# Performance work log

Hardware: AMD Instinct MI355X
Metric: run time of the kernel (lower is better)

The kernel has to match this reference:

```python
import jax, jax.numpy as jnp
import numpy as np
from jax import lax


def setup_inputs() -> dict:
    key = jax.random.key(0)
    kx, kw = jax.random.split(key)
    x = jax.random.normal(kx, (8, 32, 16, 160, 160), dtype=jnp.float32)
    # xavier-normal-ish init (scale irrelevant to correctness testing)
    weights = jax.random.normal(kw, (32, 32, 1, 3, 3), dtype=jnp.float32) * 0.1
    return {"x": x, "weights": weights}


def reference(x, weights):
    # per-(out_ch, in_ch) scale: mean |w| over kernel dims (2,3,4), detached
    scale = lax.stop_gradient(jnp.mean(jnp.abs(weights), axis=(2, 3, 4), keepdims=True))
    binary_no_grad = scale * jnp.sign(weights)          # {+-scale}
    clipped = jnp.clip(weights, -1.0, 1.0)
    # straight-through estimator: value = binary_no_grad, grad flows via clipped
    binary_weights = lax.stop_gradient(binary_no_grad - clipped) + clipped
    out = lax.conv_general_dilated(
        x, binary_weights,
        window_strides=(1, 1, 1),
        padding=((0, 0), (1, 1), (1, 1)),
        rhs_dilation=(1, 1, 1),
        dimension_numbers=("NCDHW", "OIDHW", "NCDHW"),
        feature_group_count=1,
    )
    return out
```

## Files before the change

kernel.cpp:

```cpp
#include <hip/hip_runtime.h>
#include <stdint.h>


typedef _Float16 half8  __attribute__((ext_vector_type(8)));
typedef float    floatx4 __attribute__((ext_vector_type(4)));

#define DHW 409600
#define HW  25600
#define RING_SLOT_B 10240
#define RING_B      40960
#define SCR_SLOT_B  20480
#define LDS_TOTAL   81920

__device__ __forceinline__ int w1s(int w1) { return w1 ^ ((w1 >> 2) & 1); }
__device__ __forceinline__ int f2v(int w1) { return ((w1 >> 1) ^ (w1 >> 3)) & 3; }

typedef const __attribute__((address_space(1))) uint32_t* gas1;
typedef __attribute__((address_space(3))) uint32_t* las3;
__device__ __forceinline__ void gld16(const void* g, void* l) {
    __builtin_amdgcn_global_load_lds((gas1)g, (las3)l, 16, 0, 0);
}
#define VMCNT(N) do { asm volatile("s_waitcnt vmcnt(" #N ")" ::: "memory"); \
                      __builtin_amdgcn_sched_barrier(0); } while (0)
__device__ __forceinline__ void barrier_raw() {
    __builtin_amdgcn_sched_barrier(0);
    asm volatile("s_waitcnt lgkmcnt(0)" ::: "memory");
    __builtin_amdgcn_s_barrier();
    __builtin_amdgcn_sched_barrier(0);
}

__global__ void bnn_wprep_kernel(const float* __restrict__ w,
                                 _Float16* __restrict__ ws) {
    const int tid = threadIdx.x;
    #pragma unroll
    for (int p4 = 0; p4 < 4; ++p4) {
        const int oi = tid * 4 + p4;
        const int o  = oi >> 5;
        const int i  = oi & 31;
        const float* wp = w + oi * 9;
        float s = 0.f;
        #pragma unroll
        for (int t = 0; t < 9; ++t) s += fabsf(wp[t]);
        s *= (1.f / 9.f);
        const int l = ((i >> 3) << 4) | (o & 15);
        const int p = o >> 4;
        const int j = i & 7;
        #pragma unroll
        for (int t = 0; t < 9; ++t) {
            const float v  = wp[t];
            const float sg = (v > 0.f) ? 1.f : ((v < 0.f) ? -1.f : 0.f);
            ws[((t * 2 + p) * 64 + l) * 8 + j] = (_Float16)(s * sg);
        }
    }
}

__global__ __launch_bounds__(320) void bnn_conv3d_dma(
        const float* __restrict__ x, const _Float16* __restrict__ ws,
        float* __restrict__ out) {
    extern __shared__ __align__(16) char lds[];

    const int tid  = threadIdx.x;
    const int lane = tid & 63;
    const int wv   = tid >> 6;

    const int bid = blockIdx.x;
    const int hc  = bid & 3;
    const int d   = (bid >> 2) & 15;
    const int n   = bid >> 6;
    const int h0  = hc * 40;

    const float* qb[4];
    {
        const int chl = lane >> 3;
        const int wl  = (lane & 7) * 4;
        #pragma unroll
        for (int q = 0; q < 4; ++q)
            qb[q] = x + (size_t)(n * 32 + q * 8 + chl) * DHW + d * HW + wv * 32 + wl;
    }

    half8 wf0[9], wf1[9];
    {
        const half8* fb = (const half8*)ws;
        #pragma unroll
        for (int t = 0; t < 9; ++t) {
            wf0[t] = fb[(t * 2 + 0) * 64 + lane];
            wf1[t] = fb[(t * 2 + 1) * 64 + lane];
        }
    }
    asm volatile("s_waitcnt vmcnt(0)" ::: "memory");
    __builtin_amdgcn_sched_barrier(0);

    const int pcell = 32 * wv + (lane >> 1);
    const int w1p   = w1s(pcell);
    const int wloc  = w1p - wv * 32;
    const int chb   = (lane & 1) * 16;
    int soff[16];
    #pragma unroll
    for (int c = 0; c < 16; ++c) {
        const int ch = chb + c;
        soff[c] = (wv * 4 + (ch >> 3)) * 1024 + ((ch & 7) * 8 + (wloc >> 2)) * 16
                + (wloc & 3) * 4;
    }
    const int f2p = f2v(pcell);
    const int rb0 = pcell * 64 + ((((lane & 1) * 2)     ^ f2p) * 16);
    const int rb1 = pcell * 64 + ((((lane & 1) * 2 + 1) ^ f2p) * 16);

    const int s16 = lane & 15, kgr = lane >> 4;
    int rdo[2][3];
    #pragma unroll
    for (int gi = 0; gi < 2; ++gi)
        #pragma unroll
        for (int kw = 0; kw < 3; ++kw) {
            int wq = (2 * wv + gi) * 16 + s16 + kw - 1;
            wq = wq < 0 ? 0 : (wq > 159 ? 159 : wq);
            rdo[gi][kw] = (w1s(wq) * 32 + ((kgr ^ f2v(wq)) * 8)) * 2;
        }
    const bool okA = (wv * 32 + s16 - 1) >= 0;
    const bool okB = (wv * 32 + 16 + s16 + 1) < 160;
    float* ob = out + (size_t)(n * 32 + s16) * DHW + d * HW + wv * 32 + kgr * 4;

    auto DMA = [&](int r) {
        int h = h0 - 1 + r; h = h < 0 ? 0 : (h > 159 ? 159 : h);
        char* dst = lds + RING_B + (r & 1) * SCR_SLOT_B + wv * 4096;
        #pragma unroll
        for (int q = 0; q < 4; ++q)
            gld16(qb[q] + h * 160, dst + q * 1024);
        __builtin_amdgcn_sched_barrier(0);
    };
    auto PACK = [&](int r) {
        const int hr = h0 - 1 + r;
        const char* sl = lds + RING_B + (r & 1) * SCR_SLOT_B;
        char* rg = lds + (r & 3) * RING_SLOT_B;
        half8 o0 = {}, o1 = {};
        if (hr >= 0 && hr < 160) {
            float f[16];
            #pragma unroll
            for (int c = 0; c < 16; ++c) f[c] = *(const float*)(sl + soff[c]);
            #pragma unroll
            for (int c = 0; c < 8; ++c) { o0[c] = (_Float16)f[c]; o1[c] = (_Float16)f[c + 8]; }
        }
        *(half8*)(rg + rb0) = o0;
        *(half8*)(rg + rb1) = o1;
    };
    auto COMPUTE = [&](int t) {
        const half8 zh = {};
        #pragma unroll
        for (int gi = 0; gi < 2; ++gi) {
            floatx4 a0 = {0.f, 0.f, 0.f, 0.f};
            floatx4 a1 = {0.f, 0.f, 0.f, 0.f};
            #pragma unroll
            for (int kh = 0; kh < 3; ++kh) {
                const char* sb = lds + ((t + kh) & 3) * RING_SLOT_B;
                #pragma unroll
                for (int kw = 0; kw < 3; ++kw) {
                    half8 a = *(const half8*)(sb + rdo[gi][kw]);
                    if (gi == 0 && kw == 0) a = okA ? a : zh;
                    if (gi == 1 && kw == 2) a = okB ? a : zh;
                    const int tp = kh * 3 + kw;
                    a0 = __builtin_amdgcn_mfma_f32_16x16x32_f16(a, wf0[tp], a0, 0, 0, 0);
                    a1 = __builtin_amdgcn_mfma_f32_16x16x32_f16(a, wf1[tp], a1, 0, 0, 0);
                }
            }
            float* op = ob + (size_t)(h0 + t) * 160 + gi * 16;
            *(floatx4*)op = a0;
            *(floatx4*)(op + (size_t)16 * DHW) = a1;
        }
    };

    DMA(0); DMA(1);
    VMCNT(4);  PACK(0);
    barrier_raw(); DMA(2);
    VMCNT(4);  PACK(1);
    barrier_raw(); DMA(3);
    VMCNT(4);  PACK(2); barrier_raw(); DMA(4); COMPUTE(0);
    VMCNT(8);  PACK(3); barrier_raw(); DMA(5); COMPUTE(1);
    for (int t = 2; t <= 37; ++t) {
        VMCNT(12); PACK(t + 2); barrier_raw(); DMA(t + 4); COMPUTE(t);
    }
    VMCNT(12); PACK(40); barrier_raw(); COMPUTE(38);
    VMCNT(8);  PACK(41); barrier_raw(); COMPUTE(39);
}

extern "C" void kernel_launch(void* const* d_in, const int* in_sizes, int n_in,
                              void* d_out, int out_size, void* d_ws, size_t ws_size,
                              hipStream_t stream) {
    const float* x = (const float*)d_in[0];
    const float* w = (const float*)d_in[1];
    float* out = (float*)d_out;
    _Float16* ws = (_Float16*)d_ws;
    bnn_wprep_kernel<<<dim3(1), dim3(256), 0, stream>>>(w, ws);
    (void)hipFuncSetAttribute((const void*)&bnn_conv3d_dma,
                              hipFuncAttributeMaxDynamicSharedMemorySize, LDS_TOTAL);
    bnn_conv3d_dma<<<dim3(512), dim3(320), LDS_TOTAL, stream>>>(x, ws, out);
}
```

Measured before the change: 188.7 us.

## Fuse weight binarization into conv kernel and halve grid with taller row tiles

Removes the separate single-block weight-prep kernel. Each conv block now binarizes the weights itself into LDS while its first input-row DMAs are in flight, then loads its MFMA weight fragments from LDS. The grid is halved to 256 blocks, each covering 80 output rows instead of 40, which cuts halo row reloads and per-block prologue cost. The trade-offs are redundant weight preparation in every block and fewer resident blocks per CU, so less latency hiding.

```diff
diff --git a/kernel.cpp b/kernel.cpp
--- a/kernel.cpp
+++ b/kernel.cpp
@@ -29,45 +29,20 @@
     __builtin_amdgcn_sched_barrier(0);
 }
 
-__global__ void bnn_wprep_kernel(const float* __restrict__ w,
-                                 _Float16* __restrict__ ws) {
-    const int tid = threadIdx.x;
-    #pragma unroll
-    for (int p4 = 0; p4 < 4; ++p4) {
-        const int oi = tid * 4 + p4;
-        const int o  = oi >> 5;
-        const int i  = oi & 31;
-        const float* wp = w + oi * 9;
-        float s = 0.f;
-        #pragma unroll
-        for (int t = 0; t < 9; ++t) s += fabsf(wp[t]);
-        s *= (1.f / 9.f);
-        const int l = ((i >> 3) << 4) | (o & 15);
-        const int p = o >> 4;
-        const int j = i & 7;
-        #pragma unroll
-        for (int t = 0; t < 9; ++t) {
-            const float v  = wp[t];
-            const float sg = (v > 0.f) ? 1.f : ((v < 0.f) ? -1.f : 0.f);
-            ws[((t * 2 + p) * 64 + l) * 8 + j] = (_Float16)(s * sg);
-        }
-    }
-}
-
 __global__ __launch_bounds__(320) void bnn_conv3d_dma(
-        const float* __restrict__ x, const _Float16* __restrict__ ws,
+        const float* __restrict__ x, const float* __restrict__ w,
         float* __restrict__ out) {
-    extern __shared__ __align__(16) char lds[];
+    __shared__ __align__(16) char lds[LDS_TOTAL];
 
     const int tid  = threadIdx.x;
     const int lane = tid & 63;
     const int wv   = tid >> 6;
 
     const int bid = blockIdx.x;
-    const int hc  = bid & 3;
-    const int d   = (bid >> 2) & 15;
-    const int n   = bid >> 6;
-    const int h0  = hc * 40;
+    const int hc  = bid & 1;
+    const int d   = (bid >> 1) & 15;
+    const int n   = bid >> 5;
+    const int h0  = hc * 80;
 
     const float* qb[4];
     {
@@ -78,17 +53,53 @@
             qb[q] = x + (size_t)(n * 32 + q * 8 + chl) * DHW + d * HW + wv * 32 + wl;
     }
 
+    auto DMA = [&](int r) {
+        int h = h0 - 1 + r; h = h < 0 ? 0 : (h > 159 ? 159 : h);
+        char* dst = lds + RING_B + (r & 1) * SCR_SLOT_B + wv * 4096;
+        #pragma unroll
+        for (int q = 0; q < 4; ++q)
+            gld16(qb[q] + h * 160, dst + q * 1024);
+        __builtin_amdgcn_sched_barrier(0);
+    };
+
+    DMA(0); DMA(1);
+
+    {
+        _Float16* wl16 = (_Float16*)lds;
+        if (tid < 256) {
+            #pragma unroll
+            for (int p4 = 0; p4 < 4; ++p4) {
+                const int oi = tid * 4 + p4;
+                const int o  = oi >> 5;
+                const int i  = oi & 31;
+                const float* wp = w + oi * 9;
+                float s = 0.f;
+                #pragma unroll
+                for (int t = 0; t < 9; ++t) s += fabsf(wp[t]);
+                s *= (1.f / 9.f);
+                const int l = ((i >> 3) << 4) | (o & 15);
+                const int p = o >> 4;
+                const int j = i & 7;
+                #pragma unroll
+                for (int t = 0; t < 9; ++t) {
+                    const float v  = wp[t];
+                    const float sg = (v > 0.f) ? 1.f : ((v < 0.f) ? -1.f : 0.f);
+                    wl16[((t * 2 + p) * 64 + l) * 8 + j] = (_Float16)(s * sg);
+                }
+            }
+        }
+    }
+    barrier_raw();
     half8 wf0[9], wf1[9];
     {
-        const half8* fb = (const half8*)ws;
+        const half8* fb = (const half8*)lds;
         #pragma unroll
         for (int t = 0; t < 9; ++t) {
             wf0[t] = fb[(t * 2 + 0) * 64 + lane];
             wf1[t] = fb[(t * 2 + 1) * 64 + lane];
         }
     }
-    asm volatile("s_waitcnt vmcnt(0)" ::: "memory");
-    __builtin_amdgcn_sched_barrier(0);
+    barrier_raw();
 
     const int pcell = 32 * wv + (lane >> 1);
     const int w1p   = w1s(pcell);
@@ -119,14 +130,6 @@
     const bool okB = (wv * 32 + 16 + s16 + 1) < 160;
     float* ob = out + (size_t)(n * 32 + s16) * DHW + d * HW + wv * 32 + kgr * 4;
 
-    auto DMA = [&](int r) {
-        int h = h0 - 1 + r; h = h < 0 ? 0 : (h > 159 ? 159 : h);
-        char* dst = lds + RING_B + (r & 1) * SCR_SLOT_B + wv * 4096;
-        #pragma unroll
-        for (int q = 0; q < 4; ++q)
-            gld16(qb[q] + h * 160, dst + q * 1024);
-        __builtin_amdgcn_sched_barrier(0);
-    };
     auto PACK = [&](int r) {
         const int hr = h0 - 1 + r;
         const char* sl = lds + RING_B + (r & 1) * SCR_SLOT_B;
@@ -167,18 +170,15 @@
         }
     };
 
-    DMA(0); DMA(1);
-    VMCNT(4);  PACK(0);
-    barrier_raw(); DMA(2);
-    VMCNT(4);  PACK(1);
-    barrier_raw(); DMA(3);
+    VMCNT(4);  PACK(0); barrier_raw(); DMA(2);
+    VMCNT(4);  PACK(1); barrier_raw(); DMA(3);
     VMCNT(4);  PACK(2); barrier_raw(); DMA(4); COMPUTE(0);
     VMCNT(8);  PACK(3); barrier_raw(); DMA(5); COMPUTE(1);
-    for (int t = 2; t <= 37; ++t) {
+    for (int t = 2; t <= 77; ++t) {
         VMCNT(12); PACK(t + 2); barrier_raw(); DMA(t + 4); COMPUTE(t);
     }
-    VMCNT(12); PACK(40); barrier_raw(); COMPUTE(38);
-    VMCNT(8);  PACK(41); barrier_raw(); COMPUTE(39);
+    VMCNT(12); PACK(80); barrier_raw(); COMPUTE(78);
+    VMCNT(8);  PACK(81); barrier_raw(); COMPUTE(79);
 }
 
 extern "C" void kernel_launch(void* const* d_in, const int* in_sizes, int n_in,
@@ -187,9 +187,5 @@
     const float* x = (const float*)d_in[0];
     const float* w = (const float*)d_in[1];
     float* out = (float*)d_out;
-    _Float16* ws = (_Float16*)d_ws;
-    bnn_wprep_kernel<<<dim3(1), dim3(256), 0, stream>>>(w, ws);
-    (void)hipFuncSetAttribute((const void*)&bnn_conv3d_dma,
-                              hipFuncAttributeMaxDynamicSharedMemorySize, LDS_TOTAL);
-    bnn_conv3d_dma<<<dim3(512), dim3(320), LDS_TOTAL, stream>>>(x, ws, out);
+    bnn_conv3d_dma<<<dim3(256), dim3(320), 0, stream>>>(x, w, out);
 }
```

Result: no change. 186.4 us (-1.2%).
